# Optimization experiments

Hardware: AMD Instinct MI355X
Metric: run time of the kernel (lower is better)

Reference implementation:

```python
import jax, jax.numpy as jnp
import numpy as np

B, S, D, I, L, H, F = 4, 512, 768, 64, 2, 12, 3072
DH = D // H
LN_EPS = 1e-12


def setup_inputs() -> dict:
    key = jax.random.key(0)
    ks = jax.random.split(key, 24)
    nrm = lambda k, sh, s=0.02: jax.random.normal(k, sh, jnp.float32) * s
    return {
        'hs0': nrm(ks[0], (B, S, D), 1.0),
        'hs1': nrm(ks[1], (B, S, D), 1.0),
        'hs2': nrm(ks[2], (B, S, D), 1.0),
        'Wq': nrm(ks[3], (L, D, D)), 'bq': jnp.zeros((L, D), jnp.float32),
        'Wk': nrm(ks[4], (L, D, D)), 'bk': jnp.zeros((L, D), jnp.float32),
        'Wv': nrm(ks[5], (L, D, D)), 'bv': jnp.zeros((L, D), jnp.float32),
        'Wo': nrm(ks[6], (L, D, D)), 'bo': jnp.zeros((L, D), jnp.float32),
        'ln1_g': jnp.ones((L, D), jnp.float32), 'ln1_b': jnp.zeros((L, D), jnp.float32),
        'W1': nrm(ks[7], (L, D, F)), 'b1': jnp.zeros((L, F), jnp.float32),
        'W2': nrm(ks[8], (L, F, D)), 'b2': jnp.zeros((L, D), jnp.float32),
        'ln2_g': jnp.ones((L, D), jnp.float32), 'ln2_b': jnp.zeros((L, D), jnp.float32),
        'zero_context': nrm(ks[9], (D,), 1.0),
        'ck2tok_mask': jax.random.uniform(ks[10], (B, I, S)) > 0.7,  # True = token excluded from span
        'span_size_ids': jax.random.randint(ks[11], (B, I), 0, 10),
    }


def _ln(x, g, b):
    m = jnp.mean(x, axis=-1, keepdims=True)
    v = jnp.mean((x - m) ** 2, axis=-1, keepdims=True)
    return (x - m) * jax.lax.rsqrt(v + LN_EPS) * g + b


def _forward(hs0, hs1, Wq, bq, Wk, bk, Wv, bv, Wo, bo, ln1_g, ln1_b,
             W1, b1, W2, b2, ln2_g, ln2_b, zero_context, mask):
    # mask: [B,I,S] bool, True = excluded token
    zero_indic = jnp.all(mask, axis=-1)                 # [B,I] spans with no valid token
    mask = mask & ~zero_indic[:, :, None]               # unmask degenerate rows (replaced at end)
    # masked max pooling (init aggregation) -- [B,I,S,D] intermediate, traffic-bound
    pooled = jnp.max(jnp.where(mask[..., None], -jnp.inf, hs0[:, None, :, :]), axis=2)  # [B,I,D]
    ext = (mask.astype(jnp.float32) * -10000.0)[:, None, :, :]  # [B,1,I,S] extended attn mask
    q = pooled
    hs_list = (hs0, hs1)
    inv_sqrt_dh = np.float32(1.0 / np.sqrt(DH))
    for i in range(L):
        hs = hs_list[i]
        qh = (q @ Wq[i] + bq[i]).reshape(B, I, H, DH).transpose(0, 2, 1, 3)   # [B,H,I,DH]
        kh = (hs @ Wk[i] + bk[i]).reshape(B, S, H, DH).transpose(0, 2, 1, 3)  # [B,H,S,DH]
        vh = (hs @ Wv[i] + bv[i]).reshape(B, S, H, DH).transpose(0, 2, 1, 3)
        scores = jnp.einsum('bhid,bhsd->bhis', qh, kh) * inv_sqrt_dh + ext
        attn = jax.nn.softmax(scores, axis=-1)
        ctx = jnp.einsum('bhis,bhsd->bhid', attn, vh).transpose(0, 2, 1, 3).reshape(B, I, D)
        q = _ln(q + ctx @ Wo[i] + bo[i], ln1_g[i], ln1_b[i])
        ffn = jax.nn.gelu(q @ W1[i] + b1[i], approximate=False) @ W2[i] + b2[i]
        q = _ln(q + ffn, ln2_g[i], ln2_b[i])
    # zero-context substitution for empty spans
    return jnp.where(zero_indic[..., None], zero_context, q)


def reference(hs0, hs1, hs2, Wq, bq, Wk, bk, Wv, bv, Wo, bo, ln1_g, ln1_b,
              W1, b1, W2, b2, ln2_g, ln2_b, zero_context, ck2tok_mask, span_size_ids):
    # hs2 is the last entry of the (num_layers+1) slice; query layers 0..L-1 attend hs0..hs1.
    # span_size_ids unused since use_init_size_emb=False.
    del hs2, span_size_ids
    return _forward(hs0, hs1, Wq, bq, Wk, bk, Wv, bv, Wo, bo, ln1_g, ln1_b,
                    W1, b1, W2, b2, ln2_g, ln2_b, zero_context, ck2tok_mask)
```

## Files before the change

### kernel.cpp

```cpp
#include <hip/hip_runtime.h>
#include <hip/hip_bf16.h>
#include <math.h>

#define BB 4
#define SS 512
#define DD 768
#define II 64
#define LL 2
#define HH 12
#define FF 3072

using short8 = __attribute__((ext_vector_type(8))) short;
using f32x4  = __attribute__((ext_vector_type(4))) float;

__device__ __forceinline__ unsigned short f2bf(float x) {
  return __builtin_bit_cast(unsigned short, __float2bfloat16(x));
}

__device__ __forceinline__ void gload_lds16(const void* g, void* l) {
  __builtin_amdgcn_global_load_lds((const __attribute__((address_space(1))) unsigned int*)g,
                                   (__attribute__((address_space(3))) unsigned int*)l, 16, 0, 0);
}

__global__ __launch_bounds__(256) void cast2_kernel(const float* __restrict__ a, const float* __restrict__ b,
                                                    unsigned short* __restrict__ oa, unsigned short* __restrict__ ob) {
  int idx = blockIdx.x * 256 + threadIdx.x;
  float4 va = ((const float4*)a)[idx];
  float4 vb = ((const float4*)b)[idx];
  union { unsigned short u[4]; uint2 v; } pa, pb;
  pa.u[0] = f2bf(va.x); pa.u[1] = f2bf(va.y); pa.u[2] = f2bf(va.z); pa.u[3] = f2bf(va.w);
  pb.u[0] = f2bf(vb.x); pb.u[1] = f2bf(vb.y); pb.u[2] = f2bf(vb.z); pb.u[3] = f2bf(vb.w);
  ((uint2*)oa)[idx] = pa.v;
  ((uint2*)ob)[idx] = pb.v;
}

struct TC { const float* s[6]; };

__global__ __launch_bounds__(256) void tcast_all(TC src, unsigned short* __restrict__ WT4,
                                                 unsigned short* __restrict__ W1T,
                                                 unsigned short* __restrict__ W2T) {
  __shared__ float tile[32][33];
  int z = blockIdx.z;
  const float* Ws; unsigned short* WTs; int K, N, n0, k0;
  if (z < 8) {
    if (blockIdx.x >= 24) return;
    int widx = z >> 1, l = z & 1;
    Ws = src.s[widx] + (size_t)l * DD * DD;
    WTs = WT4 + ((size_t)widx * 2 + l) * DD * DD;
    K = DD; N = DD; n0 = blockIdx.x * 32; k0 = blockIdx.y * 32;
  } else if (z < 10) {
    int l = z - 8;
    Ws = src.s[4] + (size_t)l * DD * FF;
    WTs = W1T + (size_t)l * FF * DD;
    K = DD; N = FF; n0 = blockIdx.x * 32; k0 = blockIdx.y * 32;
  } else {
    int l = z - 10;
    Ws = src.s[5] + (size_t)l * FF * DD;
    WTs = W2T + (size_t)l * DD * FF;
    K = FF; N = DD; n0 = blockIdx.y * 32; k0 = blockIdx.x * 32;
  }
  int tx = threadIdx.x, ty = threadIdx.y;
  #pragma unroll
  for (int r = 0; r < 4; ++r) tile[ty + 8 * r][tx] = Ws[(size_t)(k0 + ty + 8 * r) * N + (n0 + tx)];
  __syncthreads();
  #pragma unroll
  for (int r = 0; r < 4; ++r) WTs[(size_t)(n0 + ty + 8 * r) * K + (k0 + tx)] = f2bf(tile[tx][ty + 8 * r]);
}

__global__ __launch_bounds__(256) void pool_kernel(const float* __restrict__ hs0, const int* __restrict__ mask,
                                                   int* __restrict__ zi, float* __restrict__ qf,
                                                   unsigned short* __restrict__ qb,
                                                   unsigned long long* __restrict__ pmask) {
  __shared__ float eadd[SS];
  int bi = blockIdx.x;
  int b = bi >> 6, dz = blockIdx.y, t = threadIdx.x, w = t >> 6;
  const int* mrow = mask + (size_t)bi * SS;
  int m0v = mrow[t], m1v = mrow[t + 256];
  eadd[t] = m0v ? -__builtin_inff() : 0.0f;
  eadd[t + 256] = m1v ? -__builtin_inff() : 0.0f;
  int incl = (m0v == 0) | (m1v == 0);
  int any = __syncthreads_or(incl);
  int z = !any;
  if (dz == 0) {
    unsigned long long w0 = __ballot(z || (m0v == 0));
    unsigned long long w1 = __ballot(z || (m1v == 0));
    if ((t & 63) == 0) {
      pmask[bi * 8 + w] = w0;
      pmask[bi * 8 + 4 + w] = w1;
      if (t == 0) zi[bi] = z;
    }
  }
  const float* hb = hs0 + (size_t)b * SS * DD + dz * 256 + t;
  float m[8];
  #pragma unroll
  for (int j = 0; j < 8; ++j) m[j] = -3.4e38f;
  for (int s0 = 0; s0 < SS; s0 += 8) {
    #pragma unroll
    for (int j = 0; j < 8; ++j)
      m[j] = fmaxf(m[j], hb[(size_t)(s0 + j) * DD] + eadd[s0 + j]);
  }
  float mm = fmaxf(fmaxf(fmaxf(m[0], m[1]), fmaxf(m[2], m[3])),
                   fmaxf(fmaxf(m[4], m[5]), fmaxf(m[6], m[7])));
  size_t o = (size_t)bi * DD + dz * 256 + t;
  qf[o] = mm;
  qb[o] = f2bf(mm);
}

struct GB { const unsigned short* A; const unsigned short* Bt; const float* bias; void* C;
            int M; int N; int rowbias; };

template <int GELU, int OUTBF>
__global__ __launch_bounds__(256) void gemm_nt(GB g0, GB g1, GB g2, GB g3, int K) {
  __shared__ unsigned short Al[128 * 64];
  __shared__ unsigned short Bl[128 * 64];
  GB g = (blockIdx.z == 0) ? g0 : (blockIdx.z == 1) ? g1 : (blockIdx.z == 2) ? g2 : g3;
  int bm = blockIdx.x, bn = blockIdx.y;
  if (blockIdx.z & 1) { bm = blockIdx.y; bn = blockIdx.x; }
  if (bm * 128 >= g.M) return;
  int t = threadIdx.x, w = t >> 6, lane = t & 63;
  int hi = lane >> 4, lo = lane & 15;
  int wr = w >> 1, wc = w & 1;
  f32x4 acc[4][4] = {};
  const char* Abase = (const char*)g.A + (size_t)(bm * 128) * (size_t)K * 2;
  const char* Bbase = (const char*)g.Bt + (size_t)(bn * 128) * (size_t)K * 2;
  int rowbytes = K * 2;
  int KT = K >> 6;
  for (int kt = 0; kt < KT; ++kt) {
    int k0b = kt * 128;
    #pragma unroll
    for (int c = 0; c < 4; ++c) {
      int base = (c * 4 + w) << 10;
      int o = base + lane * 16;
      int row = o >> 7, cb = o & 127;
      int scb = cb ^ ((row & 7) << 4);
      gload_lds16(Abase + (size_t)row * rowbytes + (k0b + scb), (char*)Al + base);
      gload_lds16(Bbase + (size_t)row * rowbytes + (k0b + scb), (char*)Bl + base);
    }
    __syncthreads();
    #pragma unroll
    for (int kk = 0; kk < 2; ++kk) {
      short8 av[4], bv_[4];
      #pragma unroll
      for (int mi = 0; mi < 4; ++mi) {
        int r = wr * 64 + mi * 16 + lo;
        av[mi] = *(const short8*)((const char*)Al + r * 128 + ((kk * 64 + hi * 16) ^ ((r & 7) << 4)));
      }
      #pragma unroll
      for (int ni = 0; ni < 4; ++ni) {
        int r = wc * 64 + ni * 16 + lo;
        bv_[ni] = *(const short8*)((const char*)Bl + r * 128 + ((kk * 64 + hi * 16) ^ ((r & 7) << 4)));
      }
      #pragma unroll
      for (int mi = 0; mi < 4; ++mi)
        #pragma unroll
        for (int ni = 0; ni < 4; ++ni)
          acc[mi][ni] = __builtin_amdgcn_mfma_f32_16x16x32_bf16(av[mi], bv_[ni], acc[mi][ni], 0, 0, 0);
    }
    __syncthreads();
  }
  int mbase = bm * 128 + wr * 64;
  int nbase = bn * 128 + wc * 64;
  #pragma unroll
  for (int mi = 0; mi < 4; ++mi)
    #pragma unroll
    for (int ni = 0; ni < 4; ++ni)
      #pragma unroll
      for (int r = 0; r < 4; ++r) {
        int gm = mbase + mi * 16 + hi * 4 + r;
        int gn = nbase + ni * 16 + lo;
        float v = acc[mi][ni][r] + (g.rowbias ? g.bias[gm] : g.bias[gn]);
        if (GELU) v = 0.5f * v * (1.0f + erff(v * 0.70710678118654752f));
        if (OUTBF) ((unsigned short*)g.C)[(size_t)gm * g.N + gn] = f2bf(v);
        else       ((float*)g.C)[(size_t)gm * g.N + gn] = v;
      }
}

template <int GELU, int OUTBF, int PARTIAL>
__global__ __launch_bounds__(256) void gemm_sk(GB g, int K, int kLen) {
  __shared__ unsigned short Al[2][64 * 64];
  __shared__ unsigned short Bl[2][64 * 64];
  int bm = blockIdx.x, bn = blockIdx.y, bz = blockIdx.z;
  int t = threadIdx.x, w = t >> 6, lane = t & 63;
  int hi = lane >> 4, lo = lane & 15;
  int wr = w >> 1, wc = w & 1;
  f32x4 acc[2][2] = {};
  size_t rb = (size_t)K * 2;
  const char* Abase = (const char*)g.A + (size_t)(bm * 64) * rb + (size_t)bz * kLen * 2;
  const char* Bbase = (const char*)g.Bt + (size_t)(bn * 64) * rb + (size_t)bz * kLen * 2;
  int KT = kLen >> 6;
  auto STAGE = [&](int buf, int kt) {
    int k0b = kt * 128;
    #pragma unroll
    for (int c = 0; c < 2; ++c) {
      int base = (c * 4 + w) << 10;
      int o = base + lane * 16;
      int row = o >> 7, cb = o & 127;
      int scb = cb ^ ((row & 7) << 4);
      gload_lds16(Abase + (size_t)row * rb + (k0b + scb), (char*)Al[buf] + base);
      gload_lds16(Bbase + (size_t)row * rb + (k0b + scb), (char*)Bl[buf] + base);
    }
  };
  STAGE(0, 0);
  asm volatile("s_waitcnt vmcnt(0)" ::: "memory");
  __builtin_amdgcn_s_barrier();
  int cur = 0;
  for (int kt = 0; kt < KT; ++kt) {
    if (kt + 1 < KT) STAGE(cur ^ 1, kt + 1);
    #pragma unroll
    for (int kk = 0; kk < 2; ++kk) {
      short8 av[2], bv_[2];
      #pragma unroll
      for (int mi = 0; mi < 2; ++mi) {
        int r = wr * 32 + mi * 16 + lo;
        av[mi] = *(const short8*)((const char*)Al[cur] + r * 128 + ((kk * 64 + hi * 16) ^ ((r & 7) << 4)));
      }
      #pragma unroll
      for (int ni = 0; ni < 2; ++ni) {
        int r = wc * 32 + ni * 16 + lo;
        bv_[ni] = *(const short8*)((const char*)Bl[cur] + r * 128 + ((kk * 64 + hi * 16) ^ ((r & 7) << 4)));
      }
      #pragma unroll
      for (int mi = 0; mi < 2; ++mi)
        #pragma unroll
        for (int ni = 0; ni < 2; ++ni)
          acc[mi][ni] = __builtin_amdgcn_mfma_f32_16x16x32_bf16(av[mi], bv_[ni], acc[mi][ni], 0, 0, 0);
    }
    if (kt + 1 < KT) {
      asm volatile("s_waitcnt vmcnt(0)" ::: "memory");
      __builtin_amdgcn_s_barrier();
      cur ^= 1;
    }
  }
  int mbase = bm * 64 + wr * 32;
  int nbase = bn * 64 + wc * 32;
  #pragma unroll
  for (int mi = 0; mi < 2; ++mi)
    #pragma unroll
    for (int ni = 0; ni < 2; ++ni)
      #pragma unroll
      for (int r = 0; r < 4; ++r) {
        int gm = mbase + mi * 16 + hi * 4 + r;
        int gn = nbase + ni * 16 + lo;
        if (PARTIAL) {
          ((float*)g.C)[((size_t)bz * g.M + gm) * g.N + gn] = acc[mi][ni][r];
        } else {
          float v = acc[mi][ni][r] + g.bias[gn];
          if (GELU) v = 0.5f * v * (1.0f + erff(v * 0.70710678118654752f));
          if (OUTBF) ((unsigned short*)g.C)[(size_t)gm * g.N + gn] = f2bf(v);
          else       ((float*)g.C)[(size_t)gm * g.N + gn] = v;
        }
      }
}

#define ATTN_LDS 145664
__global__ __launch_bounds__(256) void attn_kernel(
    const unsigned short* __restrict__ qbuf, const unsigned short* __restrict__ WqTl,
    const float* __restrict__ bql, const unsigned short* __restrict__ khb,
    const unsigned short* __restrict__ vTall, const unsigned long long* __restrict__ pmask,
    unsigned short* __restrict__ ctx) {
  extern __shared__ char lds[];
  char* Qd = lds;
  char* KP = lds + 8192;
  char* Vd = lds + 8192 + 65536;
  unsigned long long* pm = (unsigned long long*)(lds + 139264);
  float* red  = (float*)(lds + 143360);
  float* red2 = (float*)(lds + 144384);
  float* rnv  = (float*)(lds + 145408);
  int bh = blockIdx.x;
  int b = bh / HH, h = bh - b * HH;
  int t = threadIdx.x, w = t >> 6, l = t & 63, hi = l >> 4, lo = l & 15;
  int o16 = l * 16, ro = o16 >> 7, cb = o16 & 127;

  const char* vsrc = (const char*)vTall + (size_t)(h * 64) * 4096 + (size_t)b * 1024;
  #pragma unroll
  for (int rr = 0; rr < 16; ++rr) {
    int rv = w * 16 + rr;
    gload_lds16(vsrc + (size_t)rv * 4096 + ((l * 16) ^ ((rv & 7) << 4)), Vd + rv * 1024);
  }
  if (w == 0) {
    const char* psrc = (const char*)pmask + (size_t)b * 4096;
    #pragma unroll
    for (int c = 0; c < 4; ++c) gload_lds16(psrc + c * 1024 + l * 16, (char*)pm + c * 1024);
  }

  const char* Aq = (const char*)qbuf + (size_t)(b * II) * 1536;
  const char* Bq = (const char*)WqTl + (size_t)(h * 64) * 1536;
  f32x4 qacc[4] = {};
  #pragma unroll
  for (int cc = 0; cc < 2; ++cc) {
    int ch = w * 2 + cc, row = ch * 8 + ro;
    int scb = cb ^ ((row & 7) << 4);
    gload_lds16(Aq + (size_t)row * 1536 + scb, KP + ch * 1024);
    gload_lds16(Bq + (size_t)row * 1536 + scb, KP + 8192 + ch * 1024);
  }
  __syncthreads();
  for (int kt = 0; kt < 12; ++kt) {
    int cur = (kt & 1) * 16384;
    if (kt < 11) {
      int nxt = ((kt + 1) & 1) * 16384;
      int kb = (kt + 1) * 128;
      #pragma unroll
      for (int cc = 0; cc < 2; ++cc) {
        int ch = w * 2 + cc, row = ch * 8 + ro;
        int scb = kb + (cb ^ ((row & 7) << 4));
        gload_lds16(Aq + (size_t)row * 1536 + scb, KP + nxt + ch * 1024);
        gload_lds16(Bq + (size_t)row * 1536 + scb, KP + nxt + 8192 + ch * 1024);
      }
    }
    #pragma unroll
    for (int kk = 0; kk < 2; ++kk) {
      int ra = w * 16 + lo;
      short8 av = *(const short8*)(KP + cur + ra * 128 + ((kk * 64 + hi * 16) ^ ((ra & 7) << 4)));
      #pragma unroll
      for (int ni = 0; ni < 4; ++ni) {
        int rb2 = ni * 16 + lo;
        short8 bv = *(const short8*)(KP + cur + 8192 + rb2 * 128 + ((kk * 64 + hi * 16) ^ ((rb2 & 7) << 4)));
        qacc[ni] = __builtin_amdgcn_mfma_f32_16x16x32_bf16(av, bv, qacc[ni], 0, 0, 0);
      }
    }
    __syncthreads();
  }
  #pragma unroll
  for (int ni = 0; ni < 4; ++ni)
    #pragma unroll
    for (int r = 0; r < 4; ++r) {
      int row = w * 16 + hi * 4 + r, col = ni * 16 + lo;
      float v = qacc[ni][r] + bql[h * 64 + col];
      *(unsigned short*)(Qd + row * 128 + ((col * 2) ^ ((row & 7) << 4))) = f2bf(v);
    }
  const char* Ks = (const char*)khb + (size_t)(b * SS) * 1536 + h * 128;
  #pragma unroll
  for (int cc = 0; cc < 16; ++cc) {
    int ch = w * 16 + cc, row = ch * 8 + ro;
    int scb = cb ^ ((row & 7) << 4);
    gload_lds16(Ks + (size_t)row * 1536 + scb, KP + ch * 1024);
  }
  __syncthreads();

  f32x4 acc[4][8] = {};
  #pragma unroll
  for (int kk = 0; kk < 2; ++kk) {
    short8 av[4];
    #pragma unroll
    for (int mi = 0; mi < 4; ++mi) {
      int ra = mi * 16 + lo;
      av[mi] = *(const short8*)(Qd + ra * 128 + ((kk * 64 + hi * 16) ^ ((ra & 7) << 4)));
    }
    #pragma unroll
    for (int ni = 0; ni < 8; ++ni) {
      int rk = w * 128 + ni * 16 + lo;
      short8 bv = *(const short8*)(KP + rk * 128 + ((kk * 64 + hi * 16) ^ ((rk & 7) << 4)));
      #pragma unroll
      for (int mi = 0; mi < 4; ++mi)
        acc[mi][ni] = __builtin_amdgcn_mfma_f32_16x16x32_bf16(av[mi], bv, acc[mi][ni], 0, 0, 0);
    }
  }
  #pragma unroll
  for (int mi = 0; mi < 4; ++mi)
    #pragma unroll
    for (int r = 0; r < 4; ++r) {
      float m = acc[mi][0][r];
      #pragma unroll
      for (int ni = 1; ni < 8; ++ni) m = fmaxf(m, acc[mi][ni][r]);
      #pragma unroll
      for (int xm = 1; xm <= 8; xm <<= 1) m = fmaxf(m, __shfl_xor(m, xm));
      if (lo == 0) red[(mi * 16 + hi * 4 + r) * 4 + w] = m;
    }
  __syncthreads();
  #pragma unroll
  for (int mi = 0; mi < 4; ++mi)
    #pragma unroll
    for (int r = 0; r < 4; ++r) {
      int row = mi * 16 + hi * 4 + r;
      float4 rm4 = *(const float4*)&red[row * 4];
      float gm = fmaxf(fmaxf(rm4.x, rm4.y), fmaxf(rm4.z, rm4.w));
      unsigned long long w0 = pm[row * 8 + w * 2 + 0];
      unsigned long long w1 = pm[row * 8 + w * 2 + 1];
      float s = 0.f;
      #pragma unroll
      for (int ni = 0; ni < 8; ++ni) {
        int sl = ni * 16 + lo;
        unsigned long long word = (sl < 64) ? w0 : w1;
        float in = ((word >> (sl & 63)) & 1ull) ? 1.0f : 0.0f;
        float e = __expf((acc[mi][ni][r] - gm) * 0.125f) * in;
        s += e;
        int sbyte = w * 256 + ni * 32 + lo * 2;
        *(unsigned short*)(KP + row * 1024 + (sbyte ^ ((row & 7) << 4))) = f2bf(e);
      }
      #pragma unroll
      for (int xm = 1; xm <= 8; xm <<= 1) s += __shfl_xor(s, xm);
      if (lo == 0) red2[row * 4 + w] = s;
    }
  __syncthreads();
  if (w == 0 && lo == 0) {
    #pragma unroll
    for (int mi = 0; mi < 4; ++mi)
      #pragma unroll
      for (int r = 0; r < 4; ++r) {
        int row = mi * 16 + hi * 4 + r;
        float4 s4 = *(const float4*)&red2[row * 4];
        rnv[row] = 1.0f / ((s4.x + s4.y) + (s4.z + s4.w));
      }
  }
  __syncthreads();
  f32x4 pacc[4] = {};
  for (int kk = 0; kk < 16; ++kk) {
    int rv = w * 16 + lo;
    short8 bv = *(const short8*)(Vd + rv * 1024 + ((kk * 64 + hi * 16) ^ ((rv & 7) << 4)));
    #pragma unroll
    for (int mi = 0; mi < 4; ++mi) {
      int ra = mi * 16 + lo;
      short8 av = *(const short8*)(KP + ra * 1024 + ((kk * 64 + hi * 16) ^ ((ra & 7) << 4)));
      pacc[mi] = __builtin_amdgcn_mfma_f32_16x16x32_bf16(av, bv, pacc[mi], 0, 0, 0);
    }
  }
  #pragma unroll
  for (int mi = 0; mi < 4; ++mi)
    #pragma unroll
    for (int r = 0; r < 4; ++r) {
      int row = mi * 16 + hi * 4 + r;
      ctx[(size_t)(b * II + row) * DD + h * 64 + w * 16 + lo] = f2bf(pacc[mi][r] * rnv[row]);
    }
}

template <int FINAL, int NP>
__global__ __launch_bounds__(256) void ln_kernel(const float* __restrict__ x, const float* __restrict__ y,
                                                 const float* __restrict__ gb,
                                                 const float* __restrict__ g, const float* __restrict__ bb,
                                                 float* __restrict__ qf, unsigned short* __restrict__ qb,
                                                 const int* __restrict__ zi, const float* __restrict__ zc,
                                                 float* __restrict__ out) {
  __shared__ float r1[4], r2[4];
  const int MN = BB * II * DD;
  int r = blockIdx.x, t = threadIdx.x;
  size_t o = (size_t)r * DD;
  float v0 = x[o + t] + gb[t];
  float v1 = x[o + t + 256] + gb[t + 256];
  float v2 = x[o + t + 512] + gb[t + 512];
  #pragma unroll
  for (int p = 0; p < NP; ++p) {
    size_t po = (size_t)p * MN + o;
    v0 += y[po + t];
    v1 += y[po + t + 256];
    v2 += y[po + t + 512];
  }
  float s = v0 + v1 + v2, ss = v0 * v0 + v1 * v1 + v2 * v2;
  #pragma unroll
  for (int o2 = 32; o2; o2 >>= 1) { s += __shfl_xor(s, o2); ss += __shfl_xor(ss, o2); }
  if ((t & 63) == 0) { r1[t >> 6] = s; r2[t >> 6] = ss; }
  __syncthreads();
  s = r1[0] + r1[1] + r1[2] + r1[3];
  ss = r2[0] + r2[1] + r2[2] + r2[3];
  float mean = s * (1.0f / DD);
  float var = ss * (1.0f / DD) - mean * mean;
  float inv = rsqrtf(var + 1e-12f);
  float w0 = (v0 - mean) * inv * g[t] + bb[t];
  float w1 = (v1 - mean) * inv * g[t + 256] + bb[t + 256];
  float w2 = (v2 - mean) * inv * g[t + 512] + bb[t + 512];
  if (FINAL) {
    int z = zi[r];
    out[o + t] = z ? zc[t] : w0;
    out[o + t + 256] = z ? zc[t + 256] : w1;
    out[o + t + 512] = z ? zc[t + 512] : w2;
  } else {
    qf[o + t] = w0; qf[o + t + 256] = w1; qf[o + t + 512] = w2;
    qb[o + t] = f2bf(w0); qb[o + t + 256] = f2bf(w1); qb[o + t + 512] = f2bf(w2);
  }
}

extern "C" void kernel_launch(void* const* d_in, const int* in_sizes, int n_in,
                              void* d_out, int out_size, void* d_ws, size_t ws_size,
                              hipStream_t stream) {
  (void)in_sizes; (void)n_in; (void)out_size; (void)ws_size;
  const float* hs0 = (const float*)d_in[0];
  const float* hs1 = (const float*)d_in[1];
  const float* Wq  = (const float*)d_in[3];
  const float* bq  = (const float*)d_in[4];
  const float* Wk  = (const float*)d_in[5];
  const float* bk  = (const float*)d_in[6];
  const float* Wv  = (const float*)d_in[7];
  const float* bv  = (const float*)d_in[8];
  const float* Wo  = (const float*)d_in[9];
  const float* bo  = (const float*)d_in[10];
  const float* ln1g = (const float*)d_in[11];
  const float* ln1b = (const float*)d_in[12];
  const float* W1  = (const float*)d_in[13];
  const float* b1  = (const float*)d_in[14];
  const float* W2  = (const float*)d_in[15];
  const float* b2  = (const float*)d_in[16];
  const float* ln2g = (const float*)d_in[17];
  const float* ln2b = (const float*)d_in[18];
  const float* zc  = (const float*)d_in[19];
  const int*   mask = (const int*)d_in[20];

  char* ws = (char*)d_ws;
  size_t off = 0;
  auto alloc = [&](size_t bytes) { size_t o = off; off += (bytes + 255) & ~(size_t)255; return o; };

  unsigned short* WT4 = (unsigned short*)(ws + alloc((size_t)4 * LL * DD * DD * 2));
  unsigned short* W1T = (unsigned short*)(ws + alloc((size_t)LL * FF * DD * 2));
  unsigned short* W2T = (unsigned short*)(ws + alloc((size_t)LL * DD * FF * 2));
  unsigned short* hsb = (unsigned short*)(ws + alloc((size_t)2 * BB * SS * DD * 2));
  float*          qf  = (float*)(ws + alloc((size_t)BB * II * DD * 4));
  unsigned short* qb  = (unsigned short*)(ws + alloc((size_t)BB * II * DD * 2));
  unsigned short* khb = (unsigned short*)(ws + alloc((size_t)LL * BB * SS * DD * 2));
  unsigned short* vTall = (unsigned short*)(ws + alloc((size_t)LL * DD * BB * SS * 2));
  unsigned short* ctxb = (unsigned short*)(ws + alloc((size_t)BB * II * DD * 2));
  float*          att_o = (float*)(ws + alloc((size_t)2 * BB * II * DD * 4));
  unsigned short* ffh = (unsigned short*)(ws + alloc((size_t)BB * II * FF * 2));
  float*          ffo = (float*)(ws + alloc((size_t)4 * BB * II * DD * 4));
  unsigned long long* pmask = (unsigned long long*)(ws + alloc((size_t)BB * II * 8 * 8));
  int*            zib = (int*)(ws + alloc((size_t)BB * II * 4));

  unsigned short* WqT = WT4 + 0 * (size_t)LL * DD * DD;
  unsigned short* WkT = WT4 + 1 * (size_t)LL * DD * DD;
  unsigned short* WvT = WT4 + 2 * (size_t)LL * DD * DD;
  unsigned short* WoT = WT4 + 3 * (size_t)LL * DD * DD;

  (void)hipFuncSetAttribute((const void*)attn_kernel,
                            hipFuncAttributeMaxDynamicSharedMemorySize, ATTN_LDS);

  dim3 tb(32, 8);
  TC tc = { { Wq, Wk, Wv, Wo, W1, W2 } };
  tcast_all<<<dim3(96, 24, 12), tb, 0, stream>>>(tc, WT4, W1T, W2T);
  cast2_kernel<<<(BB * SS * DD / 4) / 256, 256, 0, stream>>>(hs0, hs1, hsb, hsb + (size_t)BB * SS * DD);
  pool_kernel<<<dim3(BB * II, 3), 256, 0, stream>>>(hs0, mask, zib, qf, qb, pmask);

  {
    const unsigned short* h0 = hsb;
    const unsigned short* h1 = hsb + (size_t)BB * SS * DD;
    GB gK0 = { h0, WkT, bk, khb, BB * SS, DD, 0 };
    GB gV0 = { WvT, h0, bv, vTall, DD, BB * SS, 1 };
    GB gK1 = { h1, WkT + (size_t)DD * DD, bk + DD, khb + (size_t)BB * SS * DD, BB * SS, DD, 0 };
    GB gV1 = { WvT + (size_t)DD * DD, h1, bv + DD, vTall + (size_t)DD * BB * SS, DD, BB * SS, 1 };
    gemm_nt<0, 1><<<dim3(16, 6, 4), 256, 0, stream>>>(gK0, gV0, gK1, gV1, DD);
  }

  for (int l = 0; l < LL; ++l) {
    const unsigned short* khl = khb + (size_t)l * BB * SS * DD;
    const unsigned short* vTl = vTall + (size_t)l * DD * BB * SS;
    attn_kernel<<<dim3(BB * HH), 256, ATTN_LDS, stream>>>(
        qb, WqT + (size_t)l * DD * DD, bq + l * DD, khl, vTl, pmask, ctxb);
    GB gO = { ctxb, WoT + (size_t)l * DD * DD, nullptr, att_o, BB * II, DD, 0 };
    gemm_sk<0, 0, 1><<<dim3(4, 12, 2), 256, 0, stream>>>(gO, DD, DD / 2);
    ln_kernel<0, 2><<<BB * II, 256, 0, stream>>>(qf, att_o, bo + l * DD,
                                                 ln1g + l * DD, ln1b + l * DD, qf, qb,
                                                 nullptr, nullptr, nullptr);
    GB gF1 = { qb, W1T + (size_t)l * FF * DD, b1 + l * FF, ffh, BB * II, FF, 0 };
    gemm_sk<1, 1, 0><<<dim3(4, FF / 64, 1), 256, 0, stream>>>(gF1, DD, DD);
    GB gF2 = { ffh, W2T + (size_t)l * DD * FF, nullptr, ffo, BB * II, DD, 0 };
    gemm_sk<0, 0, 1><<<dim3(4, 12, 4), 256, 0, stream>>>(gF2, FF, FF / 4);
    if (l == 0)
      ln_kernel<0, 4><<<BB * II, 256, 0, stream>>>(qf, ffo, b2 + l * DD,
                                                   ln2g + l * DD, ln2b + l * DD, qf, qb,
                                                   nullptr, nullptr, nullptr);
    else
      ln_kernel<1, 4><<<BB * II, 256, 0, stream>>>(qf, ffo, b2 + l * DD,
                                                   ln2g + l * DD, ln2b + l * DD, nullptr, nullptr,
                                                   zib, zc, (float*)d_out);
  }
}
```

Before: 179.5 us.

## Merge prep kernels into one launch and double-buffer gemm_nt LDS tiles

Combines the weight transpose-cast, hidden-state cast and masked max pooling into a single flat-grid prep kernel. This removes two launches and the gaps between them, and drops the idle blocks the old 3D grid wasted on the square weights. The K/V projection GEMM now double-buffers its A/B LDS tiles, so the next tile's global-to-LDS loads are issued before the MFMA work on the current tile, with one barrier per step. LDS use per block doubles to 64KB, which may lower occupancy.

```diff
diff --git a/kernel.cpp b/kernel.cpp
--- a/kernel.cpp
+++ b/kernel.cpp
@@ -22,88 +22,88 @@
                                    (__attribute__((address_space(3))) unsigned int*)l, 16, 0, 0);
 }
 
-__global__ __launch_bounds__(256) void cast2_kernel(const float* __restrict__ a, const float* __restrict__ b,
-                                                    unsigned short* __restrict__ oa, unsigned short* __restrict__ ob) {
-  int idx = blockIdx.x * 256 + threadIdx.x;
-  float4 va = ((const float4*)a)[idx];
-  float4 vb = ((const float4*)b)[idx];
-  union { unsigned short u[4]; uint2 v; } pa, pb;
-  pa.u[0] = f2bf(va.x); pa.u[1] = f2bf(va.y); pa.u[2] = f2bf(va.z); pa.u[3] = f2bf(va.w);
-  pb.u[0] = f2bf(vb.x); pb.u[1] = f2bf(vb.y); pb.u[2] = f2bf(vb.z); pb.u[3] = f2bf(vb.w);
-  ((uint2*)oa)[idx] = pa.v;
-  ((uint2*)ob)[idx] = pb.v;
-}
-
 struct TC { const float* s[6]; };
 
-__global__ __launch_bounds__(256) void tcast_all(TC src, unsigned short* __restrict__ WT4,
-                                                 unsigned short* __restrict__ W1T,
-                                                 unsigned short* __restrict__ W2T) {
+__global__ __launch_bounds__(256) void prep_kernel(
+    TC src, unsigned short* __restrict__ WT4, unsigned short* __restrict__ W1T,
+    unsigned short* __restrict__ W2T,
+    const float* __restrict__ hs0, const float* __restrict__ hs1,
+    unsigned short* __restrict__ hsb0, unsigned short* __restrict__ hsb1,
+    const int* __restrict__ mask, int* __restrict__ zi, float* __restrict__ qf,
+    unsigned short* __restrict__ qb, unsigned long long* __restrict__ pmask) {
   __shared__ float tile[32][33];
-  int z = blockIdx.z;
-  const float* Ws; unsigned short* WTs; int K, N, n0, k0;
-  if (z < 8) {
-    if (blockIdx.x >= 24) return;
-    int widx = z >> 1, l = z & 1;
-    Ws = src.s[widx] + (size_t)l * DD * DD;
-    WTs = WT4 + ((size_t)widx * 2 + l) * DD * DD;
-    K = DD; N = DD; n0 = blockIdx.x * 32; k0 = blockIdx.y * 32;
-  } else if (z < 10) {
-    int l = z - 8;
-    Ws = src.s[4] + (size_t)l * DD * FF;
-    WTs = W1T + (size_t)l * FF * DD;
-    K = DD; N = FF; n0 = blockIdx.x * 32; k0 = blockIdx.y * 32;
+  __shared__ float eadd[SS];
+  int id = blockIdx.x;
+  int t = threadIdx.x;
+  if (id < 13824) {
+    const float* Ws; unsigned short* WTs; int K, N, n0, k0;
+    if (id < 4608) {
+      int z = id / 576, rem = id - z * 576;
+      int widx = z >> 1, l = z & 1;
+      Ws = src.s[widx] + (size_t)l * DD * DD;
+      WTs = WT4 + ((size_t)widx * 2 + l) * DD * DD;
+      K = DD; N = DD; n0 = (rem % 24) * 32; k0 = (rem / 24) * 32;
+    } else if (id < 9216) {
+      int j = id - 4608, l = j / 2304, rem = j - l * 2304;
+      Ws = src.s[4] + (size_t)l * DD * FF;
+      WTs = W1T + (size_t)l * FF * DD;
+      K = DD; N = FF; n0 = (rem % 96) * 32; k0 = (rem / 96) * 32;
+    } else {
+      int j = id - 9216, l = j / 2304, rem = j - l * 2304;
+      Ws = src.s[5] + (size_t)l * FF * DD;
+      WTs = W2T + (size_t)l * DD * FF;
+      K = FF; N = DD; n0 = (rem % 24) * 32; k0 = (rem / 24) * 32;
+    }
+    int tx = t & 31, ty = t >> 5;
+    #pragma unroll
+    for (int r = 0; r < 4; ++r) tile[ty + 8 * r][tx] = Ws[(size_t)(k0 + ty + 8 * r) * N + (n0 + tx)];
+    __syncthreads();
+    #pragma unroll
+    for (int r = 0; r < 4; ++r) WTs[(size_t)(n0 + ty + 8 * r) * K + (k0 + tx)] = f2bf(tile[tx][ty + 8 * r]);
+  } else if (id < 15360) {
+    int idx = (id - 13824) * 256 + t;
+    float4 va = ((const float4*)hs0)[idx];
+    float4 vb = ((const float4*)hs1)[idx];
+    union { unsigned short u[4]; uint2 v; } pa, pb;
+    pa.u[0] = f2bf(va.x); pa.u[1] = f2bf(va.y); pa.u[2] = f2bf(va.z); pa.u[3] = f2bf(va.w);
+    pb.u[0] = f2bf(vb.x); pb.u[1] = f2bf(vb.y); pb.u[2] = f2bf(vb.z); pb.u[3] = f2bf(vb.w);
+    ((uint2*)hsb0)[idx] = pa.v;
+    ((uint2*)hsb1)[idx] = pb.v;
   } else {
-    int l = z - 10;
-    Ws = src.s[5] + (size_t)l * FF * DD;
-    WTs = W2T + (size_t)l * DD * FF;
-    K = FF; N = DD; n0 = blockIdx.y * 32; k0 = blockIdx.x * 32;
-  }
-  int tx = threadIdx.x, ty = threadIdx.y;
-  #pragma unroll
-  for (int r = 0; r < 4; ++r) tile[ty + 8 * r][tx] = Ws[(size_t)(k0 + ty + 8 * r) * N + (n0 + tx)];
-  __syncthreads();
-  #pragma unroll
-  for (int r = 0; r < 4; ++r) WTs[(size_t)(n0 + ty + 8 * r) * K + (k0 + tx)] = f2bf(tile[tx][ty + 8 * r]);
-}
-
-__global__ __launch_bounds__(256) void pool_kernel(const float* __restrict__ hs0, const int* __restrict__ mask,
-                                                   int* __restrict__ zi, float* __restrict__ qf,
-                                                   unsigned short* __restrict__ qb,
-                                                   unsigned long long* __restrict__ pmask) {
-  __shared__ float eadd[SS];
-  int bi = blockIdx.x;
-  int b = bi >> 6, dz = blockIdx.y, t = threadIdx.x, w = t >> 6;
-  const int* mrow = mask + (size_t)bi * SS;
-  int m0v = mrow[t], m1v = mrow[t + 256];
-  eadd[t] = m0v ? -__builtin_inff() : 0.0f;
-  eadd[t + 256] = m1v ? -__builtin_inff() : 0.0f;
-  int incl = (m0v == 0) | (m1v == 0);
-  int any = __syncthreads_or(incl);
-  int z = !any;
-  if (dz == 0) {
-    unsigned long long w0 = __ballot(z || (m0v == 0));
-    unsigned long long w1 = __ballot(z || (m1v == 0));
-    if ((t & 63) == 0) {
-      pmask[bi * 8 + w] = w0;
-      pmask[bi * 8 + 4 + w] = w1;
-      if (t == 0) zi[bi] = z;
-    }
-  }
-  const float* hb = hs0 + (size_t)b * SS * DD + dz * 256 + t;
-  float m[8];
-  #pragma unroll
-  for (int j = 0; j < 8; ++j) m[j] = -3.4e38f;
-  for (int s0 = 0; s0 < SS; s0 += 8) {
-    #pragma unroll
-    for (int j = 0; j < 8; ++j)
-      m[j] = fmaxf(m[j], hb[(size_t)(s0 + j) * DD] + eadd[s0 + j]);
-  }
-  float mm = fmaxf(fmaxf(fmaxf(m[0], m[1]), fmaxf(m[2], m[3])),
-                   fmaxf(fmaxf(m[4], m[5]), fmaxf(m[6], m[7])));
-  size_t o = (size_t)bi * DD + dz * 256 + t;
-  qf[o] = mm;
-  qb[o] = f2bf(mm);
+    int j = id - 15360;
+    int bi = j & 255, dz = j >> 8;
+    int b = bi >> 6, w = t >> 6;
+    const int* mrow = mask + (size_t)bi * SS;
+    int m0v = mrow[t], m1v = mrow[t + 256];
+    eadd[t] = m0v ? -__builtin_inff() : 0.0f;
+    eadd[t + 256] = m1v ? -__builtin_inff() : 0.0f;
+    int incl = (m0v == 0) | (m1v == 0);
+    int any = __syncthreads_or(incl);
+    int z = !any;
+    if (dz == 0) {
+      unsigned long long w0 = __ballot(z || (m0v == 0));
+      unsigned long long w1 = __ballot(z || (m1v == 0));
+      if ((t & 63) == 0) {
+        pmask[bi * 8 + w] = w0;
+        pmask[bi * 8 + 4 + w] = w1;
+        if (t == 0) zi[bi] = z;
+      }
+    }
+    const float* hb = hs0 + (size_t)b * SS * DD + dz * 256 + t;
+    float m[8];
+    #pragma unroll
+    for (int jj = 0; jj < 8; ++jj) m[jj] = -3.4e38f;
+    for (int s0 = 0; s0 < SS; s0 += 8) {
+      #pragma unroll
+      for (int jj = 0; jj < 8; ++jj)
+        m[jj] = fmaxf(m[jj], hb[(size_t)(s0 + jj) * DD] + eadd[s0 + jj]);
+    }
+    float mm = fmaxf(fmaxf(fmaxf(m[0], m[1]), fmaxf(m[2], m[3])),
+                     fmaxf(fmaxf(m[4], m[5]), fmaxf(m[6], m[7])));
+    size_t o = (size_t)bi * DD + dz * 256 + t;
+    qf[o] = mm;
+    qb[o] = f2bf(mm);
+  }
 }
 
 struct GB { const unsigned short* A; const unsigned short* Bt; const float* bias; void* C;
@@ -111,8 +111,8 @@
 
 template <int GELU, int OUTBF>
 __global__ __launch_bounds__(256) void gemm_nt(GB g0, GB g1, GB g2, GB g3, int K) {
-  __shared__ unsigned short Al[128 * 64];
-  __shared__ unsigned short Bl[128 * 64];
+  __shared__ unsigned short Al[2][128 * 64];
+  __shared__ unsigned short Bl[2][128 * 64];
   GB g = (blockIdx.z == 0) ? g0 : (blockIdx.z == 1) ? g1 : (blockIdx.z == 2) ? g2 : g3;
   int bm = blockIdx.x, bn = blockIdx.y;
   if (blockIdx.z & 1) { bm = blockIdx.y; bn = blockIdx.x; }
@@ -125,7 +125,7 @@
   const char* Bbase = (const char*)g.Bt + (size_t)(bn * 128) * (size_t)K * 2;
   int rowbytes = K * 2;
   int KT = K >> 6;
-  for (int kt = 0; kt < KT; ++kt) {
+  auto STAGE = [&](int buf, int kt) {
     int k0b = kt * 128;
     #pragma unroll
     for (int c = 0; c < 4; ++c) {
@@ -133,22 +133,28 @@
       int o = base + lane * 16;
       int row = o >> 7, cb = o & 127;
       int scb = cb ^ ((row & 7) << 4);
-      gload_lds16(Abase + (size_t)row * rowbytes + (k0b + scb), (char*)Al + base);
-      gload_lds16(Bbase + (size_t)row * rowbytes + (k0b + scb), (char*)Bl + base);
-    }
-    __syncthreads();
+      gload_lds16(Abase + (size_t)row * rowbytes + (k0b + scb), (char*)Al[buf] + base);
+      gload_lds16(Bbase + (size_t)row * rowbytes + (k0b + scb), (char*)Bl[buf] + base);
+    }
+  };
+  STAGE(0, 0);
+  asm volatile("s_waitcnt vmcnt(0)" ::: "memory");
+  __builtin_amdgcn_s_barrier();
+  int cur = 0;
+  for (int kt = 0; kt < KT; ++kt) {
+    if (kt + 1 < KT) STAGE(cur ^ 1, kt + 1);
     #pragma unroll
     for (int kk = 0; kk < 2; ++kk) {
       short8 av[4], bv_[4];
       #pragma unroll
       for (int mi = 0; mi < 4; ++mi) {
         int r = wr * 64 + mi * 16 + lo;
-        av[mi] = *(const short8*)((const char*)Al + r * 128 + ((kk * 64 + hi * 16) ^ ((r & 7) << 4)));
+        av[mi] = *(const short8*)((const char*)Al[cur] + r * 128 + ((kk * 64 + hi * 16) ^ ((r & 7) << 4)));
       }
       #pragma unroll
       for (int ni = 0; ni < 4; ++ni) {
         int r = wc * 64 + ni * 16 + lo;
-        bv_[ni] = *(const short8*)((const char*)Bl + r * 128 + ((kk * 64 + hi * 16) ^ ((r & 7) << 4)));
+        bv_[ni] = *(const short8*)((const char*)Bl[cur] + r * 128 + ((kk * 64 + hi * 16) ^ ((r & 7) << 4)));
       }
       #pragma unroll
       for (int mi = 0; mi < 4; ++mi)
@@ -156,7 +162,11 @@
         for (int ni = 0; ni < 4; ++ni)
           acc[mi][ni] = __builtin_amdgcn_mfma_f32_16x16x32_bf16(av[mi], bv_[ni], acc[mi][ni], 0, 0, 0);
     }
-    __syncthreads();
+    if (kt + 1 < KT) {
+      asm volatile("s_waitcnt vmcnt(0)" ::: "memory");
+      __builtin_amdgcn_s_barrier();
+      cur ^= 1;
+    }
   }
   int mbase = bm * 128 + wr * 64;
   int nbase = bn * 128 + wc * 64;
@@ -520,11 +530,10 @@
   (void)hipFuncSetAttribute((const void*)attn_kernel,
                             hipFuncAttributeMaxDynamicSharedMemorySize, ATTN_LDS);
 
-  dim3 tb(32, 8);
   TC tc = { { Wq, Wk, Wv, Wo, W1, W2 } };
-  tcast_all<<<dim3(96, 24, 12), tb, 0, stream>>>(tc, WT4, W1T, W2T);
-  cast2_kernel<<<(BB * SS * DD / 4) / 256, 256, 0, stream>>>(hs0, hs1, hsb, hsb + (size_t)BB * SS * DD);
-  pool_kernel<<<dim3(BB * II, 3), 256, 0, stream>>>(hs0, mask, zib, qf, qb, pmask);
+  prep_kernel<<<16128, 256, 0, stream>>>(tc, WT4, W1T, W2T, hs0, hs1,
+                                         hsb, hsb + (size_t)BB * SS * DD,
+                                         mask, zib, qf, qb, pmask);
 
   {
     const unsigned short* h0 = hsb;
```

New measurement: 181.0 us. About the same (+0.8%).

## Fuse post-attention LayerNorm into FFN1 GEMM prologue

Applied to the files above, without the earlier changes.

Replaces the separate LN1 kernel plus FFN1 GEMM with one kernel. Each block recomputes the residual-add and LayerNorm for its 64 rows into LDS as bf16, then runs the W1 GEMM with GELU. Block column 0 writes the fp32 normalized output to a new buffer, which the LN2 kernel now reads. This removes one launch and the qb round trip to global memory, at the cost of repeating the LN work in each of the 48 column blocks and holding a large LDS footprint (about 112 KB) per block.

```diff
diff --git a/kernel.cpp b/kernel.cpp
--- a/kernel.cpp
+++ b/kernel.cpp
@@ -249,6 +249,110 @@
           if (OUTBF) ((unsigned short*)g.C)[(size_t)gm * g.N + gn] = f2bf(v);
           else       ((float*)g.C)[(size_t)gm * g.N + gn] = v;
         }
+      }
+}
+
+#define FFN1_LDS (98304 + 16384)
+__global__ __launch_bounds__(256) void ffn1_kernel(
+    const float* __restrict__ qf_in, const float* __restrict__ att_o, const float* __restrict__ bo,
+    const float* __restrict__ g, const float* __restrict__ bb, float* __restrict__ qf_out,
+    const unsigned short* __restrict__ W1T, const float* __restrict__ b1,
+    unsigned short* __restrict__ ffh) {
+  extern __shared__ char shm[];
+  char* Adata = shm;
+  char* Bl = shm + 98304;
+  const int MN = BB * II * DD;
+  int bm = blockIdx.x, bn = blockIdx.y;
+  int t = threadIdx.x, w = t >> 6, lane = t & 63;
+  int hi = lane >> 4, lo = lane & 15;
+  int wr = w >> 1, wc = w & 1;
+
+  for (int i = 0; i < 16; ++i) {
+    int rloc = w + 4 * i;
+    int row = bm * 64 + rloc;
+    size_t o = (size_t)row * DD;
+    float v[12];
+    float s = 0.f, ss = 0.f;
+    #pragma unroll
+    for (int j = 0; j < 12; ++j) {
+      int c = lane + 64 * j;
+      float x = qf_in[o + c] + bo[c] + att_o[o + c] + att_o[MN + o + c];
+      v[j] = x; s += x; ss += x * x;
+    }
+    #pragma unroll
+    for (int o2 = 32; o2; o2 >>= 1) { s += __shfl_xor(s, o2); ss += __shfl_xor(ss, o2); }
+    float mean = s * (1.0f / DD);
+    float var = ss * (1.0f / DD) - mean * mean;
+    float inv = rsqrtf(var + 1e-12f);
+    #pragma unroll
+    for (int j = 0; j < 12; ++j) {
+      int c = lane + 64 * j;
+      float wv = (v[j] - mean) * inv * g[c] + bb[c];
+      *(unsigned short*)(Adata + j * 8192 + rloc * 128 + ((lane * 2) ^ ((rloc & 7) << 4))) = f2bf(wv);
+      if (bn == 0) qf_out[o + c] = wv;
+    }
+  }
+  __syncthreads();
+
+  f32x4 acc[2][2] = {};
+  size_t rb = (size_t)DD * 2;
+  const char* Bbase = (const char*)W1T + (size_t)(bn * 64) * rb;
+  auto STAGEB = [&](int buf, int kt) {
+    int k0b = kt * 128;
+    #pragma unroll
+    for (int c = 0; c < 2; ++c) {
+      int base = (c * 4 + w) << 10;
+      int o = base + lane * 16;
+      int row = o >> 7, cb = o & 127;
+      int scb = cb ^ ((row & 7) << 4);
+      gload_lds16(Bbase + (size_t)row * rb + (k0b + scb), Bl + buf * 8192 + base);
+    }
+  };
+  STAGEB(0, 0);
+  asm volatile("s_waitcnt vmcnt(0)" ::: "memory");
+  __builtin_amdgcn_s_barrier();
+  int cur = 0;
+  for (int kt = 0; kt < 12; ++kt) {
+    if (kt + 1 < 12) STAGEB(cur ^ 1, kt + 1);
+    const char* Al = Adata + kt * 8192;
+    #pragma unroll
+    for (int kk = 0; kk < 2; ++kk) {
+      short8 av[2], bv_[2];
+      #pragma unroll
+      for (int mi = 0; mi < 2; ++mi) {
+        int r = wr * 32 + mi * 16 + lo;
+        av[mi] = *(const short8*)(Al + r * 128 + ((kk * 64 + hi * 16) ^ ((r & 7) << 4)));
+      }
+      #pragma unroll
+      for (int ni = 0; ni < 2; ++ni) {
+        int r = wc * 32 + ni * 16 + lo;
+        bv_[ni] = *(const short8*)(Bl + cur * 8192 + r * 128 + ((kk * 64 + hi * 16) ^ ((r & 7) << 4)));
+      }
+      #pragma unroll
+      for (int mi = 0; mi < 2; ++mi)
+        #pragma unroll
+        for (int ni = 0; ni < 2; ++ni)
+          acc[mi][ni] = __builtin_amdgcn_mfma_f32_16x16x32_bf16(av[mi], bv_[ni], acc[mi][ni], 0, 0, 0);
+    }
+    if (kt + 1 < 12) {
+      asm volatile("s_waitcnt vmcnt(0)" ::: "memory");
+      __builtin_amdgcn_s_barrier();
+      cur ^= 1;
+    }
+  }
+  int mbase = bm * 64 + wr * 32;
+  int nbase = bn * 64 + wc * 32;
+  #pragma unroll
+  for (int mi = 0; mi < 2; ++mi)
+    #pragma unroll
+    for (int ni = 0; ni < 2; ++ni)
+      #pragma unroll
+      for (int r = 0; r < 4; ++r) {
+        int gm = mbase + mi * 16 + hi * 4 + r;
+        int gn = nbase + ni * 16 + lo;
+        float v = acc[mi][ni][r] + b1[gn];
+        v = 0.5f * v * (1.0f + erff(v * 0.70710678118654752f));
+        ffh[(size_t)gm * FF + gn] = f2bf(v);
       }
 }
 
@@ -502,6 +606,7 @@
   unsigned short* W2T = (unsigned short*)(ws + alloc((size_t)LL * DD * FF * 2));
   unsigned short* hsb = (unsigned short*)(ws + alloc((size_t)2 * BB * SS * DD * 2));
   float*          qf  = (float*)(ws + alloc((size_t)BB * II * DD * 4));
+  float*          qf2 = (float*)(ws + alloc((size_t)BB * II * DD * 4));
   unsigned short* qb  = (unsigned short*)(ws + alloc((size_t)BB * II * DD * 2));
   unsigned short* khb = (unsigned short*)(ws + alloc((size_t)LL * BB * SS * DD * 2));
   unsigned short* vTall = (unsigned short*)(ws + alloc((size_t)LL * DD * BB * SS * 2));
@@ -519,6 +624,8 @@
 
   (void)hipFuncSetAttribute((const void*)attn_kernel,
                             hipFuncAttributeMaxDynamicSharedMemorySize, ATTN_LDS);
+  (void)hipFuncSetAttribute((const void*)ffn1_kernel,
+                            hipFuncAttributeMaxDynamicSharedMemorySize, FFN1_LDS);
 
   dim3 tb(32, 8);
   TC tc = { { Wq, Wk, Wv, Wo, W1, W2 } };
@@ -543,19 +650,17 @@
         qb, WqT + (size_t)l * DD * DD, bq + l * DD, khl, vTl, pmask, ctxb);
     GB gO = { ctxb, WoT + (size_t)l * DD * DD, nullptr, att_o, BB * II, DD, 0 };
     gemm_sk<0, 0, 1><<<dim3(4, 12, 2), 256, 0, stream>>>(gO, DD, DD / 2);
-    ln_kernel<0, 2><<<BB * II, 256, 0, stream>>>(qf, att_o, bo + l * DD,
-                                                 ln1g + l * DD, ln1b + l * DD, qf, qb,
-                                                 nullptr, nullptr, nullptr);
-    GB gF1 = { qb, W1T + (size_t)l * FF * DD, b1 + l * FF, ffh, BB * II, FF, 0 };
-    gemm_sk<1, 1, 0><<<dim3(4, FF / 64, 1), 256, 0, stream>>>(gF1, DD, DD);
+    ffn1_kernel<<<dim3(4, FF / 64), 256, FFN1_LDS, stream>>>(
+        qf, att_o, bo + l * DD, ln1g + l * DD, ln1b + l * DD, qf2,
+        W1T + (size_t)l * FF * DD, b1 + l * FF, ffh);
     GB gF2 = { ffh, W2T + (size_t)l * DD * FF, nullptr, ffo, BB * II, DD, 0 };
     gemm_sk<0, 0, 1><<<dim3(4, 12, 4), 256, 0, stream>>>(gF2, FF, FF / 4);
     if (l == 0)
-      ln_kernel<0, 4><<<BB * II, 256, 0, stream>>>(qf, ffo, b2 + l * DD,
+      ln_kernel<0, 4><<<BB * II, 256, 0, stream>>>(qf2, ffo, b2 + l * DD,
                                                    ln2g + l * DD, ln2b + l * DD, qf, qb,
                                                    nullptr, nullptr, nullptr);
     else
-      ln_kernel<1, 4><<<BB * II, 256, 0, stream>>>(qf, ffo, b2 + l * DD,
+      ln_kernel<1, 4><<<BB * II, 256, 0, stream>>>(qf2, ffo, b2 + l * DD,
                                                    ln2g + l * DD, ln2b + l * DD, nullptr, nullptr,
                                                    zib, zc, (float*)d_out);
   }
```

New measurement: 200.5 us. 1.12x slower.
